# Performance work log

Hardware: AMD Instinct MI355X
Metric: run time of the kernel (lower is better)

The kernel has to match this reference:

```python
import jax, jax.numpy as jnp
import numpy as np

N = 10000          # nodes
E = 320000         # edges (~32 neighbors/node)
HID = 128          # hidden_channels
NF = 128           # num_filters
NG = 50            # num_gaussians
NB = 6             # num_interactions
CUT = 10.0         # cutoff


def ssp(x):
    # ShiftedSoftplus: softplus(x) - log(2)
    return jax.nn.softplus(x) - jnp.log(2.0).astype(x.dtype)


def setup_inputs() -> dict:
    key = jax.random.key(0)
    ks = jax.random.split(key, 16)
    z = jax.random.randint(ks[0], (N,), 0, 100)
    pos = jax.random.uniform(ks[1], (N, 3), dtype=jnp.float32) * 5.0  # box so d < cutoff
    row = jax.random.randint(ks[2], (E,), 0, N)
    off = jax.random.randint(ks[3], (E,), 1, N)  # avoid self-loops (radius_graph excludes them)
    col = (row + off) % N
    edge_index = jnp.stack([row, col], axis=0)
    nrm = lambda k, s: 0.1 * jax.random.normal(k, s, dtype=jnp.float32)
    return {
        "z": z,
        "pos": pos,
        "edge_index": edge_index,
        "emb": nrm(ks[4], (100, HID)),
        "mlp_w1": nrm(ks[5], (NB, NG, NF)),
        "mlp_b1": jnp.zeros((NB, NF), jnp.float32),
        "mlp_w2": nrm(ks[6], (NB, NF, NF)),
        "mlp_b2": jnp.zeros((NB, NF), jnp.float32),
        "cl1_w": nrm(ks[7], (NB, HID, NF)),
        "cl2_w": nrm(ks[8], (NB, NF, HID)),
        "cl2_b": jnp.zeros((NB, HID), jnp.float32),
        "lin_w": nrm(ks[9], (NB, HID, HID)),
        "lin_b": jnp.zeros((NB, HID), jnp.float32),
        "out_w1": nrm(ks[10], (HID, HID // 2)),
        "out_b1": jnp.zeros((HID // 2,), jnp.float32),
        "out_w2": nrm(ks[11], (HID // 2, 1)),
        "out_b2": jnp.zeros((1,), jnp.float32),
    }


def schnet_fwd(z, pos, edge_index, emb, mlp_w1, mlp_b1, mlp_w2, mlp_b2,
               cl1_w, cl2_w, cl2_b, lin_w, lin_b, out_w1, out_b1, out_w2, out_b2):
    row, col = edge_index[0], edge_index[1]  # j (source), i (target)
    d = jnp.linalg.norm(pos[row] - pos[col], axis=-1)  # [E]
    offsets = jnp.linspace(0.0, CUT, NG)
    coeff = -0.5 / (offsets[1] - offsets[0]) ** 2
    edge_attr = jnp.exp(coeff * (d[:, None] - offsets) ** 2)  # [E, NG]
    C = 0.5 * (jnp.cos(d * jnp.pi / CUT) + 1.0)  # cosine cutoff [E]
    h = emb[z]  # [N, HID]
    n = h.shape[0]
    for k in range(NB):
        # per-edge filter MLP
        W = ssp(edge_attr @ mlp_w1[k] + mlp_b1[k]) @ mlp_w2[k] + mlp_b2[k]
        W = W * C[:, None]  # [E, NF]
        x = h @ cl1_w[k]  # lin1 (no bias) [N, NF]
        msg = x[row] * W  # gather + modulate
        agg = jax.ops.segment_sum(msg, col, num_segments=n)  # scatter-add to targets
        x = agg @ cl2_w[k] + cl2_b[k]  # lin2 [N, HID]
        x = ssp(x)
        x = x @ lin_w[k] + lin_b[k]  # InteractionBlock.lin
        h = h + x  # residual
    h = ssp(h @ out_w1 + out_b1)
    return h @ out_w2 + out_b2  # [N, 1]


def reference(z, pos, edge_index, emb, mlp_w1, mlp_b1, mlp_w2, mlp_b2,
              cl1_w, cl2_w, cl2_b, lin_w, lin_b, out_w1, out_b1, out_w2, out_b2):
    return schnet_fwd(z, pos, edge_index, emb, mlp_w1, mlp_b1, mlp_w2, mlp_b2,
                      cl1_w, cl2_w, cl2_b, lin_w, lin_b, out_w1, out_b1, out_w2, out_b2)
```

## Files before the change

kernel.cpp:

```cpp
#include <hip/hip_runtime.h>
#include <math.h>

#define N_NODES 10000
#define N_EDGES 320000
#define HID 128
#define NF 128
#define NG 50
#define NB 6
#define SCAN_CH 40
#define WFRAG_PER_K 24576
#define NWF_PER_MAT 32768
#define TBL_M 2048
#define DMAX 8.6602540378f

typedef __attribute__((ext_vector_type(8))) short bf16x8;
typedef __attribute__((ext_vector_type(4))) float f32x4;
typedef __attribute__((ext_vector_type(4))) unsigned int u32x4;

__device__ __forceinline__ int pi_map(int f) {
  return (f & ~31) | ((f & 15) << 1) | ((f >> 4) & 1);
}
__device__ __forceinline__ int pinv_map(int g) {
  return (g & ~31) | ((g & 1) << 4) | ((g & 31) >> 1);
}

__device__ __forceinline__ unsigned short f2bf(float f) {
  unsigned u = __float_as_uint(f);
  u += 0x7FFFu + ((u >> 16) & 1u);
  return (unsigned short)(u >> 16);
}
__device__ __forceinline__ float bf2f(unsigned short s) {
  return __uint_as_float(((unsigned)s) << 16);
}
__device__ __forceinline__ unsigned pack2f(float a, float b) {
  return ((__float_as_uint(a) + 0x8000u) >> 16) |
         ((__float_as_uint(b) + 0x8000u) & 0xFFFF0000u);
}
__device__ __forceinline__ float ssp_fast(float x) {
  float t = __expf(-fabsf(x));
  return fmaxf(x, 0.0f) + __logf(1.0f + t) - 0.69314718055994530942f;
}

__global__ __launch_bounds__(256) void k_embed(const int* __restrict__ z,
                                               const float* __restrict__ emb,
                                               float* __restrict__ h) {
  int t = blockIdx.x * 256 + threadIdx.x;
  if (t >= N_NODES * HID) return;
  int i = t >> 7, c = t & 127;
  h[t] = emb[z[i] * HID + c];
}

__global__ __launch_bounds__(256) void k_hist(const int* __restrict__ col,
                                              int* __restrict__ count) {
  int e = blockIdx.x * 256 + threadIdx.x;
  if (e < N_EDGES) atomicAdd(&count[col[e]], 1);
}

__global__ __launch_bounds__(256) void k_scan(const int* __restrict__ count,
                                              int* __restrict__ rowptr,
                                              int* __restrict__ cursor) {
  __shared__ int s_part[256];
  int t = threadIdx.x;
  int begin = t * SCAN_CH, end = min(begin + SCAN_CH, N_NODES);
  int s = 0;
  for (int i = begin; i < end; i++) s += count[i];
  s_part[t] = s;
  __syncthreads();
  for (int off = 1; off < 256; off <<= 1) {
    int v = (t >= off) ? s_part[t - off] : 0;
    __syncthreads();
    s_part[t] += v;
    __syncthreads();
  }
  int run = (t > 0) ? s_part[t - 1] : 0;
  for (int i = begin; i < end; i++) {
    rowptr[i] = run;
    cursor[i] = run;
    run += count[i];
  }
  if (t == 255) rowptr[N_NODES] = N_EDGES;
}

__global__ __launch_bounds__(256) void k_scatter(const int* __restrict__ row,
                                                 const int* __restrict__ col,
                                                 const float* __restrict__ pos,
                                                 int* __restrict__ cursor,
                                                 int2* __restrict__ sorted_ru) {
  int e = blockIdx.x * 256 + threadIdx.x;
  if (e >= N_EDGES) return;
  int c = col[e], r = row[e];
  float dx = pos[3 * r + 0] - pos[3 * c + 0];
  float dy = pos[3 * r + 1] - pos[3 * c + 1];
  float dz = pos[3 * r + 2] - pos[3 * c + 2];
  float d = sqrtf(dx * dx + dy * dy + dz * dz);
  int p = atomicAdd(&cursor[c], 1);
  float u = d * ((float)(TBL_M - 1) / DMAX);
  sorted_ru[p] = make_int2(r, __float_as_int(u));
}

__global__ __launch_bounds__(256) void k_pack(const float* __restrict__ w1,
                                              const float* __restrict__ w2,
                                              unsigned short* __restrict__ wf) {
  const float* w1k = w1 + (size_t)blockIdx.x * NG * NF;
  const float* w2k = w2 + (size_t)blockIdx.x * NF * NF;
  unsigned short* wfk = wf + (size_t)blockIdx.x * WFRAG_PER_K;
  for (int inst = threadIdx.x; inst < 3072; inst += 256) {
    int fi = inst >> 8;
    int wv = (inst >> 6) & 3;
    int lane = inst & 63;
    int r16 = lane & 15, kgrp = lane >> 4;
    bf16x8 v;
#pragma unroll
    for (int j = 0; j < 8; ++j) {
      float val;
      if (fi < 4) {
        int ncol = wv * 32 + r16 + (fi >> 1) * 16;
        int k = (fi & 1) * 32 + kgrp * 8 + j;
        val = (k < NG) ? w1k[k * NF + ncol] : 0.f;
      } else {
        int fi2 = fi - 4;
        int ncol = wv * 32 + r16 + (fi2 >> 2) * 16;
        int kpi = (fi2 & 3) * 32 + kgrp * 8 + j;
        val = w2k[pinv_map(kpi) * NF + ncol];
      }
      v[j] = (short)f2bf(val);
    }
    *(bf16x8*)&wfk[inst * 8] = v;
  }
}

__global__ __launch_bounds__(256) void k_packn(const float* __restrict__ cl1,
                                               const float* __restrict__ cl2,
                                               const float* __restrict__ lin,
                                               unsigned short* __restrict__ nwf) {
  const int mat = blockIdx.x;
  const float* src = (mat < 6) ? cl1 + (size_t)mat * HID * NF
                   : (mat < 12) ? cl2 + (size_t)(mat - 6) * NF * HID
                                : lin + (size_t)(mat - 12) * HID * HID;
  unsigned short* dst = nwf + (size_t)mat * NWF_PER_MAT;
  for (int inst = threadIdx.x; inst < 2048; inst += 256) {
    int fi = inst >> 8;
    int wv = (inst >> 6) & 3;
    int lane = inst & 63;
    int r16 = lane & 15, kgrp = lane >> 4;
    int ncol = wv * 32 + r16 + (fi >> 2) * 16;
    int kb = fi & 3;
    bf16x8 fh, fl;
#pragma unroll
    for (int j = 0; j < 8; ++j) {
      float val = src[(kb * 32 + kgrp * 8 + j) * 128 + ncol];
      unsigned short hh = f2bf(val);
      fh[j] = (short)hh;
      fl[j] = (short)f2bf(val - bf2f(hh));
    }
    *(bf16x8*)&dst[((fi * 4 + wv) * 64 + lane) * 8] = fh;
    *(bf16x8*)&dst[(((fi + 8) * 4 + wv) * 64 + lane) * 8] = fl;
  }
}

__device__ __forceinline__ void stage_hilo(unsigned short* s_hi, unsigned short* s_lo,
                                           int rr, int c4, float4 v) {
  int cs = c4 ^ ((rr & 7) << 3);
  unsigned hax = (__float_as_uint(v.x) + 0x8000u) & 0xFFFF0000u;
  unsigned hay = (__float_as_uint(v.y) + 0x8000u) & 0xFFFF0000u;
  unsigned haz = (__float_as_uint(v.z) + 0x8000u) & 0xFFFF0000u;
  unsigned haw = (__float_as_uint(v.w) + 0x8000u) & 0xFFFF0000u;
  float lx = v.x - __uint_as_float(hax);
  float ly = v.y - __uint_as_float(hay);
  float lz = v.z - __uint_as_float(haz);
  float lw = v.w - __uint_as_float(haw);
  *(uint2*)&s_hi[rr * 128 + cs] = make_uint2((hax >> 16) | hay, (haz >> 16) | haw);
  *(uint2*)&s_lo[rr * 128 + cs] = make_uint2(pack2f(lx, ly), pack2f(lz, lw));
}

__device__ __forceinline__ int swz_idx(int row, int col) {
  return row * 128 + (((col & ~7) ^ ((row & 7) << 3)) | (col & 7));
}

#define KSTEP(accA, accB, kb, BH_A, BL_A, BH_B, BL_B, rowoff)                  \
  {                                                                            \
    bf16x8 ahi = *(const bf16x8*)&s_hi[(rowoff) + (((kb) * 32 + kb0) ^ swz)];  \
    bf16x8 alo = *(const bf16x8*)&s_lo[(rowoff) + (((kb) * 32 + kb0) ^ swz)];  \
    accA = __builtin_amdgcn_mfma_f32_16x16x32_bf16(ahi, BH_A, accA, 0, 0, 0);  \
    accA = __builtin_amdgcn_mfma_f32_16x16x32_bf16(alo, BH_A, accA, 0, 0, 0);  \
    accA = __builtin_amdgcn_mfma_f32_16x16x32_bf16(ahi, BL_A, accA, 0, 0, 0);  \
    accB = __builtin_amdgcn_mfma_f32_16x16x32_bf16(ahi, BH_B, accB, 0, 0, 0);  \
    accB = __builtin_amdgcn_mfma_f32_16x16x32_bf16(alo, BH_B, accB, 0, 0, 0);  \
    accB = __builtin_amdgcn_mfma_f32_16x16x32_bf16(ahi, BL_B, accB, 0, 0, 0);  \
  }
#define MFMA_ALL()                                          \
  {                                                         \
    const int ro0 = r16 * 128;                              \
    KSTEP(a00, a01, 0, bh00, bl00, bh10, bl10, ro0);        \
    KSTEP(a00, a01, 1, bh01, bl01, bh11, bl11, ro0);        \
    KSTEP(a00, a01, 2, bh02, bl02, bh12, bl12, ro0);        \
    KSTEP(a00, a01, 3, bh03, bl03, bh13, bl13, ro0);        \
    const int ro1 = (16 + r16) * 128;                       \
    KSTEP(a10, a11, 0, bh00, bl00, bh10, bl10, ro1);        \
    KSTEP(a10, a11, 1, bh01, bl01, bh11, bl11, ro1);        \
    KSTEP(a10, a11, 2, bh02, bl02, bh12, bl12, ro1);        \
    KSTEP(a10, a11, 3, bh03, bl03, bh13, bl13, ro1);        \
  }
#define LOAD_FRAGS(wfp)                                                              \
  const bf16x8* np = (const bf16x8*)(wfp);                                           \
  const bf16x8 bh00 = np[(0 * 4 + wvid) * 64 + lane], bh01 = np[(1 * 4 + wvid) * 64 + lane], \
               bh02 = np[(2 * 4 + wvid) * 64 + lane], bh03 = np[(3 * 4 + wvid) * 64 + lane], \
               bh10 = np[(4 * 4 + wvid) * 64 + lane], bh11 = np[(5 * 4 + wvid) * 64 + lane], \
               bh12 = np[(6 * 4 + wvid) * 64 + lane], bh13 = np[(7 * 4 + wvid) * 64 + lane], \
               bl00 = np[(8 * 4 + wvid) * 64 + lane], bl01 = np[(9 * 4 + wvid) * 64 + lane], \
               bl02 = np[(10 * 4 + wvid) * 64 + lane], bl03 = np[(11 * 4 + wvid) * 64 + lane], \
               bl10 = np[(12 * 4 + wvid) * 64 + lane], bl11 = np[(13 * 4 + wvid) * 64 + lane], \
               bl12 = np[(14 * 4 + wvid) * 64 + lane], bl13 = np[(15 * 4 + wvid) * 64 + lane];

__global__ __launch_bounds__(256) void k_ngemm(const float* __restrict__ in,
                                               const unsigned short* __restrict__ wf,
                                               float* __restrict__ out,
                                               int nrows) {
  __shared__ __align__(16) float s_buf[32 * 128];
  unsigned short* s_hi = (unsigned short*)s_buf;
  unsigned short* s_lo = s_hi + 32 * 128;
  float* s_out = s_buf;

  const int tid = threadIdx.x;
  const int lane = tid & 63;
  const int wvid = tid >> 6;
  const int r16 = lane & 15;
  const int kgrp = lane >> 4;
  const int kb0 = kgrp * 8;
  const int nc0 = wvid * 32 + r16;
  const int nc1 = nc0 + 16;
  const int r0 = blockIdx.x * 32;

#pragma unroll
  for (int j = 0; j < 4; ++j) {
    int idx4 = j * 256 + tid;
    int rr = idx4 >> 5;
    int c4 = (idx4 & 31) << 2;
    float4 v = make_float4(0.f, 0.f, 0.f, 0.f);
    if (r0 + rr < nrows) v = *(const float4*)&in[(size_t)(r0 + rr) * 128 + c4];
    stage_hilo(s_hi, s_lo, rr, c4, v);
  }
  LOAD_FRAGS(wf);
  __syncthreads();

  f32x4 a00 = {0.f, 0.f, 0.f, 0.f}, a01 = a00, a10 = a00, a11 = a00;
  const int swz = (r16 & 7) << 3;
  MFMA_ALL();
  __syncthreads();

#pragma unroll
  for (int r = 0; r < 4; ++r) {
    int er0 = kgrp * 4 + r, er1 = 16 + kgrp * 4 + r;
    s_out[er0 * 128 + (nc0 ^ ((er0 & 7) << 2))] = a00[r];
    s_out[er0 * 128 + (nc1 ^ ((er0 & 7) << 2))] = a01[r];
    s_out[er1 * 128 + (nc0 ^ ((er1 & 7) << 2))] = a10[r];
    s_out[er1 * 128 + (nc1 ^ ((er1 & 7) << 2))] = a11[r];
  }
  __syncthreads();

#pragma unroll
  for (int j = 0; j < 4; ++j) {
    int idx4 = j * 256 + tid;
    int rr = idx4 >> 5;
    int c4 = (idx4 & 31) << 2;
    if (r0 + rr >= nrows) continue;
    int cs = c4 ^ ((rr & 7) << 2);
    *(float4*)&out[(size_t)(r0 + rr) * 128 + c4] = *(float4*)&s_out[rr * 128 + cs];
  }
}

__global__ __launch_bounds__(256) void k_ngemm2(const float* __restrict__ agg,
                                                const unsigned short* __restrict__ wf_cl2,
                                                const float* __restrict__ b_cl2,
                                                const unsigned short* __restrict__ wf_lin,
                                                const float* __restrict__ b_lin,
                                                float* __restrict__ h,
                                                int nrows) {
  __shared__ __align__(16) float s_buf[32 * 128];
  unsigned short* s_hi = (unsigned short*)s_buf;
  unsigned short* s_lo = s_hi + 32 * 128;
  float* s_out = s_buf;

  const int tid = threadIdx.x;
  const int lane = tid & 63;
  const int wvid = tid >> 6;
  const int r16 = lane & 15;
  const int kgrp = lane >> 4;
  const int kb0 = kgrp * 8;
  const int nc0 = wvid * 32 + r16;
  const int nc1 = nc0 + 16;
  const int r0 = blockIdx.x * 32;
  const int swz = (r16 & 7) << 3;

#pragma unroll
  for (int j = 0; j < 4; ++j) {
    int idx4 = j * 256 + tid;
    int rr = idx4 >> 5;
    int c4 = (idx4 & 31) << 2;
    float4 v = make_float4(0.f, 0.f, 0.f, 0.f);
    if (r0 + rr < nrows) v = *(const float4*)&agg[(size_t)(r0 + rr) * 128 + c4];
    stage_hilo(s_hi, s_lo, rr, c4, v);
  }
  const float bc0 = b_cl2[nc0], bc1 = b_cl2[nc1];
  const float bl0_ = b_lin[nc0], bl1_ = b_lin[nc1];
  __syncthreads();

  f32x4 a00 = {0.f, 0.f, 0.f, 0.f}, a01 = a00, a10 = a00, a11 = a00;
  {
    LOAD_FRAGS(wf_cl2);
    MFMA_ALL();
  }
  __syncthreads();

#pragma unroll
  for (int r = 0; r < 4; ++r) {
    int er0 = kgrp * 4 + r, er1 = 16 + kgrp * 4 + r;
    float t00 = ssp_fast(a00[r] + bc0);
    float t01 = ssp_fast(a01[r] + bc1);
    float t10 = ssp_fast(a10[r] + bc0);
    float t11 = ssp_fast(a11[r] + bc1);
    unsigned u;
    u = (__float_as_uint(t00) + 0x8000u) & 0xFFFF0000u;
    s_hi[swz_idx(er0, nc0)] = (unsigned short)(u >> 16);
    s_lo[swz_idx(er0, nc0)] = (unsigned short)(pack2f(t00 - __uint_as_float(u), 0.f));
    u = (__float_as_uint(t01) + 0x8000u) & 0xFFFF0000u;
    s_hi[swz_idx(er0, nc1)] = (unsigned short)(u >> 16);
    s_lo[swz_idx(er0, nc1)] = (unsigned short)(pack2f(t01 - __uint_as_float(u), 0.f));
    u = (__float_as_uint(t10) + 0x8000u) & 0xFFFF0000u;
    s_hi[swz_idx(er1, nc0)] = (unsigned short)(u >> 16);
    s_lo[swz_idx(er1, nc0)] = (unsigned short)(pack2f(t10 - __uint_as_float(u), 0.f));
    u = (__float_as_uint(t11) + 0x8000u) & 0xFFFF0000u;
    s_hi[swz_idx(er1, nc1)] = (unsigned short)(u >> 16);
    s_lo[swz_idx(er1, nc1)] = (unsigned short)(pack2f(t11 - __uint_as_float(u), 0.f));
  }
  __syncthreads();

  f32x4 c00 = {0.f, 0.f, 0.f, 0.f}, c01 = c00, c10 = c00, c11 = c00;
  {
    LOAD_FRAGS(wf_lin);
    const int ro0 = r16 * 128;
    KSTEP(c00, c01, 0, bh00, bl00, bh10, bl10, ro0);
    KSTEP(c00, c01, 1, bh01, bl01, bh11, bl11, ro0);
    KSTEP(c00, c01, 2, bh02, bl02, bh12, bl12, ro0);
    KSTEP(c00, c01, 3, bh03, bl03, bh13, bl13, ro0);
    const int ro1 = (16 + r16) * 128;
    KSTEP(c10, c11, 0, bh00, bl00, bh10, bl10, ro1);
    KSTEP(c10, c11, 1, bh01, bl01, bh11, bl11, ro1);
    KSTEP(c10, c11, 2, bh02, bl02, bh12, bl12, ro1);
    KSTEP(c10, c11, 3, bh03, bl03, bh13, bl13, ro1);
  }
  __syncthreads();

#pragma unroll
  for (int r = 0; r < 4; ++r) {
    int er0 = kgrp * 4 + r, er1 = 16 + kgrp * 4 + r;
    s_out[er0 * 128 + (nc0 ^ ((er0 & 7) << 2))] = c00[r] + bl0_;
    s_out[er0 * 128 + (nc1 ^ ((er0 & 7) << 2))] = c01[r] + bl1_;
    s_out[er1 * 128 + (nc0 ^ ((er1 & 7) << 2))] = c10[r] + bl0_;
    s_out[er1 * 128 + (nc1 ^ ((er1 & 7) << 2))] = c11[r] + bl1_;
  }
  __syncthreads();

#pragma unroll
  for (int j = 0; j < 4; ++j) {
    int idx4 = j * 256 + tid;
    int rr = idx4 >> 5;
    int c4 = (idx4 & 31) << 2;
    if (r0 + rr >= nrows) continue;
    int cs = c4 ^ ((rr & 7) << 2);
    float4 v = *(float4*)&s_out[rr * 128 + cs];
    float* dst = &h[(size_t)(r0 + rr) * 128 + c4];
    float4 o = *(const float4*)dst;
    v.x += o.x; v.y += o.y; v.z += o.z; v.w += o.w;
    *(float4*)dst = v;
  }
}

__global__ __launch_bounds__(256) void k_ngemm3(const float* __restrict__ agg,
                                                const unsigned short* __restrict__ wf_cl2,
                                                const float* __restrict__ b_cl2,
                                                const unsigned short* __restrict__ wf_lin,
                                                const float* __restrict__ b_lin,
                                                const unsigned short* __restrict__ wf_cl1n,
                                                float* __restrict__ h,
                                                float* __restrict__ x,
                                                int nrows) {
  __shared__ __align__(16) float s_buf[32 * 128];
  unsigned short* s_hi = (unsigned short*)s_buf;
  unsigned short* s_lo = s_hi + 32 * 128;
  float* s_out = s_buf;

  const int tid = threadIdx.x;
  const int lane = tid & 63;
  const int wvid = tid >> 6;
  const int r16 = lane & 15;
  const int kgrp = lane >> 4;
  const int kb0 = kgrp * 8;
  const int nc0 = wvid * 32 + r16;
  const int nc1 = nc0 + 16;
  const int r0 = blockIdx.x * 32;
  const int swz = (r16 & 7) << 3;

#pragma unroll
  for (int j = 0; j < 4; ++j) {
    int idx4 = j * 256 + tid;
    int rr = idx4 >> 5;
    int c4 = (idx4 & 31) << 2;
    float4 v = make_float4(0.f, 0.f, 0.f, 0.f);
    if (r0 + rr < nrows) v = *(const float4*)&agg[(size_t)(r0 + rr) * 128 + c4];
    stage_hilo(s_hi, s_lo, rr, c4, v);
  }
  const float bc0 = b_cl2[nc0], bc1 = b_cl2[nc1];
  const float bl0_ = b_lin[nc0], bl1_ = b_lin[nc1];
  __syncthreads();

  f32x4 a00 = {0.f, 0.f, 0.f, 0.f}, a01 = a00, a10 = a00, a11 = a00;
  {
    LOAD_FRAGS(wf_cl2);
    MFMA_ALL();
  }
  __syncthreads();

#pragma unroll
  for (int r = 0; r < 4; ++r) {
    int er0 = kgrp * 4 + r, er1 = 16 + kgrp * 4 + r;
    float t00 = ssp_fast(a00[r] + bc0);
    float t01 = ssp_fast(a01[r] + bc1);
    float t10 = ssp_fast(a10[r] + bc0);
    float t11 = ssp_fast(a11[r] + bc1);
    unsigned u;
    u = (__float_as_uint(t00) + 0x8000u) & 0xFFFF0000u;
    s_hi[swz_idx(er0, nc0)] = (unsigned short)(u >> 16);
    s_lo[swz_idx(er0, nc0)] = (unsigned short)(pack2f(t00 - __uint_as_float(u), 0.f));
    u = (__float_as_uint(t01) + 0x8000u) & 0xFFFF0000u;
    s_hi[swz_idx(er0, nc1)] = (unsigned short)(u >> 16);
    s_lo[swz_idx(er0, nc1)] = (unsigned short)(pack2f(t01 - __uint_as_float(u), 0.f));
    u = (__float_as_uint(t10) + 0x8000u) & 0xFFFF0000u;
    s_hi[swz_idx(er1, nc0)] = (unsigned short)(u >> 16);
    s_lo[swz_idx(er1, nc0)] = (unsigned short)(pack2f(t10 - __uint_as_float(u), 0.f));
    u = (__float_as_uint(t11) + 0x8000u) & 0xFFFF0000u;
    s_hi[swz_idx(er1, nc1)] = (unsigned short)(u >> 16);
    s_lo[swz_idx(er1, nc1)] = (unsigned short)(pack2f(t11 - __uint_as_float(u), 0.f));
  }
  __syncthreads();

  f32x4 c00 = {0.f, 0.f, 0.f, 0.f}, c01 = c00, c10 = c00, c11 = c00;
  {
    LOAD_FRAGS(wf_lin);
    const int ro0 = r16 * 128;
    KSTEP(c00, c01, 0, bh00, bl00, bh10, bl10, ro0);
    KSTEP(c00, c01, 1, bh01, bl01, bh11, bl11, ro0);
    KSTEP(c00, c01, 2, bh02, bl02, bh12, bl12, ro0);
    KSTEP(c00, c01, 3, bh03, bl03, bh13, bl13, ro0);
    const int ro1 = (16 + r16) * 128;
    KSTEP(c10, c11, 0, bh00, bl00, bh10, bl10, ro1);
    KSTEP(c10, c11, 1, bh01, bl01, bh11, bl11, ro1);
    KSTEP(c10, c11, 2, bh02, bl02, bh12, bl12, ro1);
    KSTEP(c10, c11, 3, bh03, bl03, bh13, bl13, ro1);
  }
  __syncthreads();

#pragma unroll
  for (int r = 0; r < 4; ++r) {
    int er0 = kgrp * 4 + r, er1 = 16 + kgrp * 4 + r;
    s_out[er0 * 128 + (nc0 ^ ((er0 & 7) << 2))] = c00[r] + bl0_;
    s_out[er0 * 128 + (nc1 ^ ((er0 & 7) << 2))] = c01[r] + bl1_;
    s_out[er1 * 128 + (nc0 ^ ((er1 & 7) << 2))] = c10[r] + bl0_;
    s_out[er1 * 128 + (nc1 ^ ((er1 & 7) << 2))] = c11[r] + bl1_;
  }
  __syncthreads();

  float4 vv[4];
#pragma unroll
  for (int j = 0; j < 4; ++j) {
    int idx4 = j * 256 + tid;
    int rr = idx4 >> 5;
    int c4 = (idx4 & 31) << 2;
    int cs = c4 ^ ((rr & 7) << 2);
    float4 v = *(float4*)&s_out[rr * 128 + cs];
    if (r0 + rr < nrows) {
      float4 o = *(const float4*)&h[(size_t)(r0 + rr) * 128 + c4];
      v.x += o.x; v.y += o.y; v.z += o.z; v.w += o.w;
    } else {
      v = make_float4(0.f, 0.f, 0.f, 0.f);
    }
    vv[j] = v;
  }
  __syncthreads();
#pragma unroll
  for (int j = 0; j < 4; ++j) {
    int idx4 = j * 256 + tid;
    int rr = idx4 >> 5;
    int c4 = (idx4 & 31) << 2;
    stage_hilo(s_hi, s_lo, rr, c4, vv[j]);
    if (r0 + rr < nrows) *(float4*)&h[(size_t)(r0 + rr) * 128 + c4] = vv[j];
  }
  __syncthreads();

  a00 = (f32x4){0.f, 0.f, 0.f, 0.f}; a01 = a00; a10 = a00; a11 = a00;
  {
    LOAD_FRAGS(wf_cl1n);
    MFMA_ALL();
  }
  __syncthreads();

#pragma unroll
  for (int r = 0; r < 4; ++r) {
    int er0 = kgrp * 4 + r, er1 = 16 + kgrp * 4 + r;
    s_out[er0 * 128 + (nc0 ^ ((er0 & 7) << 2))] = a00[r];
    s_out[er0 * 128 + (nc1 ^ ((er0 & 7) << 2))] = a01[r];
    s_out[er1 * 128 + (nc0 ^ ((er1 & 7) << 2))] = a10[r];
    s_out[er1 * 128 + (nc1 ^ ((er1 & 7) << 2))] = a11[r];
  }
  __syncthreads();

#pragma unroll
  for (int j = 0; j < 4; ++j) {
    int idx4 = j * 256 + tid;
    int rr = idx4 >> 5;
    int c4 = (idx4 & 31) << 2;
    if (r0 + rr >= nrows) continue;
    int cs = c4 ^ ((rr & 7) << 2);
    *(float4*)&x[(size_t)(r0 + rr) * 128 + c4] = *(float4*)&s_out[rr * 128 + cs];
  }
}

__global__ __launch_bounds__(256) void k_tbuild(
    const unsigned short* __restrict__ wf_all, const float* __restrict__ b1_all,
    const float* __restrict__ b2_all, float* __restrict__ T_all) {
  __shared__ __align__(16) unsigned short s_rbf[128 * 64];
  __shared__ __align__(16) unsigned short s_t1[128 * 128];
  __shared__ float s_C[128];

  const int kk = blockIdx.x >> 4;
  const int sb = blockIdx.x & 15;
  const int s0 = sb * 128;
  const unsigned short* wf = wf_all + (size_t)kk * WFRAG_PER_K;
  const float* b1 = b1_all + (size_t)kk * NF;
  const float* b2 = b2_all + (size_t)kk * NF;
  float* T = T_all + (size_t)kk * TBL_M * NF;

  const int tid = threadIdx.x;
  const int lane = tid & 63;
  const int wvid = tid >> 6;
  const int r16 = lane & 15;
  const int kgrp = lane >> 4;
  const int kb0 = kgrp * 8;
  const int nc0 = wvid * 32 + r16;
  const int nc1 = nc0 + 16;
  const int pcol = wvid * 32 + 2 * r16;

  const bf16x8* wp = (const bf16x8*)wf;
#define FR(fi) wp[((fi) * 4 + wvid) * 64 + lane]
  const bf16x8 w1_00 = FR(0), w1_10 = FR(1), w1_01 = FR(2), w1_11 = FR(3);
  const bf16x8 w2_00 = FR(4), w2_10 = FR(5), w2_20 = FR(6), w2_30 = FR(7);
  const bf16x8 w2_01 = FR(8), w2_11 = FR(9), w2_21 = FR(10), w2_31 = FR(11);
#undef FR
  const float b1n0 = b1[nc0], b1n1 = b1[nc1];
  const float b2n0 = b2[nc0], b2n1 = b2[nc1];

  {
    const int e = tid >> 1, gh = tid & 1;
    const float d = (float)(s0 + e) * (DMAX / (float)(TBL_M - 1));
    if (gh == 0) s_C[e] = 0.5f * (__cosf(d * 0.31415926535897932f) + 1.0f);
    const float step = 10.0f / 49.0f;
    const float coeff = -0.5f / (step * step);
    const int swz = (e & 7) << 3;
#pragma unroll
    for (int o = 0; o < 4; ++o) {
      int g0 = gh * 32 + o * 8;
      float vv[8];
#pragma unroll
      for (int j = 0; j < 8; ++j) {
        int g = g0 + j;
        float t = d - step * (float)g;
        vv[j] = (g < NG) ? __expf(coeff * t * t) : 0.0f;
      }
      u32x4 pk;
      pk[0] = pack2f(vv[0], vv[1]);
      pk[1] = pack2f(vv[2], vv[3]);
      pk[2] = pack2f(vv[4], vv[5]);
      pk[3] = pack2f(vv[6], vv[7]);
      *(u32x4*)&s_rbf[e * 64 + (g0 ^ swz)] = pk;
    }
  }
  __syncthreads();

  {
    const int swz = (r16 & 7) << 3;
    for (int mt = 0; mt < 8; ++mt) {
      const unsigned short* rp = &s_rbf[(mt * 16 + r16) * 64];
      bf16x8 a0 = *(const bf16x8*)&rp[(0 + kb0) ^ swz];
      bf16x8 a1 = *(const bf16x8*)&rp[(32 + kb0) ^ swz];
      f32x4 ac0 = {0.f, 0.f, 0.f, 0.f};
      f32x4 ac1 = {0.f, 0.f, 0.f, 0.f};
      ac0 = __builtin_amdgcn_mfma_f32_16x16x32_bf16(a0, w1_00, ac0, 0, 0, 0);
      ac0 = __builtin_amdgcn_mfma_f32_16x16x32_bf16(a1, w1_10, ac0, 0, 0, 0);
      ac1 = __builtin_amdgcn_mfma_f32_16x16x32_bf16(a0, w1_01, ac1, 0, 0, 0);
      ac1 = __builtin_amdgcn_mfma_f32_16x16x32_bf16(a1, w1_11, ac1, 0, 0, 0);
#pragma unroll
      for (int r = 0; r < 4; ++r) {
        int er = mt * 16 + kgrp * 4 + r;
        float v0 = ssp_fast(ac0[r] + b1n0);
        float v1 = ssp_fast(ac1[r] + b1n1);
        *(unsigned*)&s_t1[er * 128 + (pcol ^ ((er & 7) << 3))] = pack2f(v0, v1);
      }
    }
  }
  __syncthreads();

  {
    const int swz = (r16 & 7) << 3;
    for (int mt = 0; mt < 8; ++mt) {
      const unsigned short* tp = &s_t1[(mt * 16 + r16) * 128];
      bf16x8 a0 = *(const bf16x8*)&tp[(0 + kb0) ^ swz];
      bf16x8 a1 = *(const bf16x8*)&tp[(32 + kb0) ^ swz];
      bf16x8 a2 = *(const bf16x8*)&tp[(64 + kb0) ^ swz];
      bf16x8 a3 = *(const bf16x8*)&tp[(96 + kb0) ^ swz];
      f32x4 ac0 = {0.f, 0.f, 0.f, 0.f};
      f32x4 ac1 = {0.f, 0.f, 0.f, 0.f};
      ac0 = __builtin_amdgcn_mfma_f32_16x16x32_bf16(a0, w2_00, ac0, 0, 0, 0);
      ac0 = __builtin_amdgcn_mfma_f32_16x16x32_bf16(a1, w2_10, ac0, 0, 0, 0);
      ac0 = __builtin_amdgcn_mfma_f32_16x16x32_bf16(a2, w2_20, ac0, 0, 0, 0);
      ac0 = __builtin_amdgcn_mfma_f32_16x16x32_bf16(a3, w2_30, ac0, 0, 0, 0);
      ac1 = __builtin_amdgcn_mfma_f32_16x16x32_bf16(a0, w2_01, ac1, 0, 0, 0);
      ac1 = __builtin_amdgcn_mfma_f32_16x16x32_bf16(a1, w2_11, ac1, 0, 0, 0);
      ac1 = __builtin_amdgcn_mfma_f32_16x16x32_bf16(a2, w2_21, ac1, 0, 0, 0);
      ac1 = __builtin_amdgcn_mfma_f32_16x16x32_bf16(a3, w2_31, ac1, 0, 0, 0);
#pragma unroll
      for (int r = 0; r < 4; ++r) {
        int er = mt * 16 + kgrp * 4 + r;
        float Cc = s_C[er];
        float2 v = make_float2((ac0[r] + b2n0) * Cc, (ac1[r] + b2n1) * Cc);
        *(float2*)&T[(size_t)(s0 + er) * NF + pcol] = v;
      }
    }
  }
}

__global__ __launch_bounds__(256) void k_tpack(const float* __restrict__ T_all,
                                               unsigned* __restrict__ Tp_all) {
  size_t t = (size_t)blockIdx.x * 256 + threadIdx.x;
  int f = (int)(t & 127);
  size_t rem = t >> 7;
  int i = (int)(rem & (TBL_M - 1));
  int kk = (int)(rem >> 11);
  const float* T = T_all + (size_t)kk * TBL_M * NF;
  int pf = pi_map(f);
  float lo = T[(size_t)i * NF + pf];
  float hi = T[(size_t)min(i + 1, TBL_M - 1) * NF + pf];
  Tp_all[t] = pack2f(lo, hi);
}

__global__ __launch_bounds__(256) void k_aggr(const int2* __restrict__ ru,
                                              const int* __restrict__ rowptr,
                                              const unsigned* __restrict__ Tp,
                                              const float* __restrict__ x,
                                              float* __restrict__ agg) {
  __shared__ int2 s_ru[256];
  __shared__ float s_part[3 * 128];
  const int tid = threadIdx.x;
  const int wvid = tid >> 6;
  const int lane = tid & 63;
  const int f2 = lane * 2;
  const int n = blockIdx.x;
  const int beg = rowptr[n], end = rowptr[n + 1];

  float ax0 = 0.f, ay0 = 0.f, ax1 = 0.f, ay1 = 0.f;
  for (int cs = beg; cs < end; cs += 256) {
    const int cnt = min(256, end - cs);
    if (tid < cnt) s_ru[tid] = ru[cs + tid];
    __syncthreads();
    int j = wvid;
    for (; j + 4 < cnt; j += 8) {
      int2 p0 = s_ru[j];
      int2 p1 = s_ru[j + 4];
      float u0 = __int_as_float(p0.y), u1 = __int_as_float(p1.y);
      int i0 = min((int)u0, TBL_M - 2), i1 = min((int)u1, TBL_M - 2);
      float fr0 = u0 - (float)i0, fr1 = u1 - (float)i1;
      uint2 t0 = *(const uint2*)&Tp[(size_t)i0 * NF + f2];
      uint2 t1 = *(const uint2*)&Tp[(size_t)i1 * NF + f2];
      float2 x0 = *(const float2*)&x[(size_t)p0.x * NF + f2];
      float2 x1 = *(const float2*)&x[(size_t)p1.x * NF + f2];
      float lo, hi;
      lo = __uint_as_float(t0.x << 16); hi = __uint_as_float(t0.x & 0xFFFF0000u);
      ax0 = fmaf(fmaf(fr0, hi - lo, lo), x0.x, ax0);
      lo = __uint_as_float(t0.y << 16); hi = __uint_as_float(t0.y & 0xFFFF0000u);
      ay0 = fmaf(fmaf(fr0, hi - lo, lo), x0.y, ay0);
      lo = __uint_as_float(t1.x << 16); hi = __uint_as_float(t1.x & 0xFFFF0000u);
      ax1 = fmaf(fmaf(fr1, hi - lo, lo), x1.x, ax1);
      lo = __uint_as_float(t1.y << 16); hi = __uint_as_float(t1.y & 0xFFFF0000u);
      ay1 = fmaf(fmaf(fr1, hi - lo, lo), x1.y, ay1);
    }
    for (; j < cnt; j += 4) {
      int2 p0 = s_ru[j];
      float u0 = __int_as_float(p0.y);
      int i0 = min((int)u0, TBL_M - 2);
      float fr0 = u0 - (float)i0;
      uint2 t0 = *(const uint2*)&Tp[(size_t)i0 * NF + f2];
      float2 x0 = *(const float2*)&x[(size_t)p0.x * NF + f2];
      float lo, hi;
      lo = __uint_as_float(t0.x << 16); hi = __uint_as_float(t0.x & 0xFFFF0000u);
      ax0 = fmaf(fmaf(fr0, hi - lo, lo), x0.x, ax0);
      lo = __uint_as_float(t0.y << 16); hi = __uint_as_float(t0.y & 0xFFFF0000u);
      ay0 = fmaf(fmaf(fr0, hi - lo, lo), x0.y, ay0);
    }
    __syncthreads();
  }

  float fx = ax0 + ax1, fy = ay0 + ay1;
  if (wvid > 0) {
    *(float2*)&s_part[(wvid - 1) * 128 + f2] = make_float2(fx, fy);
  }
  __syncthreads();
  if (wvid == 0) {
#pragma unroll
    for (int w = 0; w < 3; ++w) {
      fx += s_part[w * 128 + f2];
      fy += s_part[w * 128 + f2 + 1];
    }
    *(float2*)&agg[(size_t)n * NF + f2] = make_float2(fx, fy);
  }
}

__global__ __launch_bounds__(256) void k_out(const float* __restrict__ h,
                                             const float* __restrict__ w1,
                                             const float* __restrict__ b1,
                                             const float* __restrict__ w2,
                                             const float* __restrict__ b2,
                                             float* __restrict__ out) {
  int wid = threadIdx.x >> 6;
  int lane = threadIdx.x & 63;
  int i = blockIdx.x * 4 + wid;
  if (i >= N_NODES) return;
  const float* __restrict__ hr = h + i * HID;
  float acc = b1[lane];
#pragma unroll 8
  for (int k = 0; k < HID; k++) acc = fmaf(hr[k], w1[k * 64 + lane], acc);
  float p = ssp_fast(acc) * w2[lane];
#pragma unroll
  for (int off = 32; off; off >>= 1) p += __shfl_down(p, off);
  if (lane == 0) out[i] = p + b2[0];
}

extern "C" void kernel_launch(void* const* d_in, const int* in_sizes, int n_in,
                              void* d_out, int out_size, void* d_ws, size_t ws_size,
                              hipStream_t stream) {
  const int* z = (const int*)d_in[0];
  const float* pos = (const float*)d_in[1];
  const int* eidx = (const int*)d_in[2];
  const float* emb = (const float*)d_in[3];
  const float* mlp_w1 = (const float*)d_in[4];
  const float* mlp_b1 = (const float*)d_in[5];
  const float* mlp_w2 = (const float*)d_in[6];
  const float* mlp_b2 = (const float*)d_in[7];
  const float* cl1_w = (const float*)d_in[8];
  const float* cl2_w = (const float*)d_in[9];
  const float* cl2_b = (const float*)d_in[10];
  const float* lin_w = (const float*)d_in[11];
  const float* lin_b = (const float*)d_in[12];
  const float* out_w1 = (const float*)d_in[13];
  const float* out_b1 = (const float*)d_in[14];
  const float* out_w2 = (const float*)d_in[15];
  const float* out_b2 = (const float*)d_in[16];
  float* out = (float*)d_out;

  float* h = (float*)d_ws;
  float* x = h + N_NODES * HID;
  float* agg = x + N_NODES * HID;
  int* count = (int*)(agg + N_NODES * HID);
  int* rowptr = count + 10240;
  int* cursor = rowptr + 10240;
  int2* sorted_ru = (int2*)(cursor + 10240);
  unsigned short* wfrag = (unsigned short*)(sorted_ru + N_EDGES);
  unsigned short* nwf = wfrag + (size_t)NB * WFRAG_PER_K;
  float* Tbl = (float*)(nwf + (size_t)18 * NWF_PER_MAT);
  unsigned* Tp = (unsigned*)(Tbl + (size_t)NB * TBL_M * NF);
  const int* row = eidx;
  const int* col = eidx + N_EDGES;

  hipMemsetAsync(count, 0, 10240 * sizeof(int), stream);
  k_hist<<<(N_EDGES + 255) / 256, 256, 0, stream>>>(col, count);
  k_scan<<<1, 256, 0, stream>>>(count, rowptr, cursor);
  k_scatter<<<(N_EDGES + 255) / 256, 256, 0, stream>>>(row, col, pos, cursor,
                                                       sorted_ru);

  k_pack<<<NB, 256, 0, stream>>>(mlp_w1, mlp_w2, wfrag);
  k_packn<<<18, 256, 0, stream>>>(cl1_w, cl2_w, lin_w, nwf);
  k_tbuild<<<NB * 16, 256, 0, stream>>>(wfrag, mlp_b1, mlp_b2, Tbl);
  k_tpack<<<(NB * TBL_M * NF) / 256, 256, 0, stream>>>(Tbl, Tp);

  k_embed<<<(N_NODES * HID + 255) / 256, 256, 0, stream>>>(z, emb, h);

  const int NGB = (N_NODES + 31) / 32;
  k_ngemm<<<NGB, 256, 0, stream>>>(h, nwf + (size_t)0 * NWF_PER_MAT, x, N_NODES);
  for (int k = 0; k < NB; k++) {
    k_aggr<<<N_NODES, 256, 0, stream>>>(sorted_ru, rowptr,
                                        Tp + (size_t)k * TBL_M * NF, x, agg);
    if (k < NB - 1) {
      k_ngemm3<<<NGB, 256, 0, stream>>>(
          agg, nwf + (size_t)(6 + k) * NWF_PER_MAT, cl2_b + (size_t)k * HID,
          nwf + (size_t)(12 + k) * NWF_PER_MAT, lin_b + (size_t)k * HID,
          nwf + (size_t)(k + 1) * NWF_PER_MAT, h, x, N_NODES);
    } else {
      k_ngemm2<<<NGB, 256, 0, stream>>>(
          agg, nwf + (size_t)(6 + k) * NWF_PER_MAT, cl2_b + (size_t)k * HID,
          nwf + (size_t)(12 + k) * NWF_PER_MAT, lin_b + (size_t)k * HID, h, N_NODES);
    }
  }

  k_out<<<(N_NODES + 3) / 4, 256, 0, stream>>>(h, out_w1, out_b1, out_w2, out_b2, out);
}
```

Measured before the change: 360.0 us.

## Store node features as bf16 for edge gather and halve GEMM row tiles

The lin1 output x is now written as packed bf16 pairs instead of fp32, so the per-edge gather in the aggregation kernel reads half the bytes per neighbour. Separately, the node GEMM kernels now process 16 rows per block instead of 32, which doubles the grid size for more parallelism across CUs. The trade-off is lower precision in the gathered features, and each block reloads the weight fragments for fewer rows.

Result: faster. 320.3 us (-11.0%).

```diff
diff --git a/kernel.cpp b/kernel.cpp
--- a/kernel.cpp
+++ b/kernel.cpp
@@ -177,10 +177,10 @@
   return row * 128 + (((col & ~7) ^ ((row & 7) << 3)) | (col & 7));
 }
 
-#define KSTEP(accA, accB, kb, BH_A, BL_A, BH_B, BL_B, rowoff)                  \
+#define KSTEP(accA, accB, kb, BH_A, BL_A, BH_B, BL_B)                          \
   {                                                                            \
-    bf16x8 ahi = *(const bf16x8*)&s_hi[(rowoff) + (((kb) * 32 + kb0) ^ swz)];  \
-    bf16x8 alo = *(const bf16x8*)&s_lo[(rowoff) + (((kb) * 32 + kb0) ^ swz)];  \
+    bf16x8 ahi = *(const bf16x8*)&s_hi[r16 * 128 + (((kb) * 32 + kb0) ^ swz)]; \
+    bf16x8 alo = *(const bf16x8*)&s_lo[r16 * 128 + (((kb) * 32 + kb0) ^ swz)]; \
     accA = __builtin_amdgcn_mfma_f32_16x16x32_bf16(ahi, BH_A, accA, 0, 0, 0);  \
     accA = __builtin_amdgcn_mfma_f32_16x16x32_bf16(alo, BH_A, accA, 0, 0, 0);  \
     accA = __builtin_amdgcn_mfma_f32_16x16x32_bf16(ahi, BL_A, accA, 0, 0, 0);  \
@@ -188,18 +188,12 @@
     accB = __builtin_amdgcn_mfma_f32_16x16x32_bf16(alo, BH_B, accB, 0, 0, 0);  \
     accB = __builtin_amdgcn_mfma_f32_16x16x32_bf16(ahi, BL_B, accB, 0, 0, 0);  \
   }
-#define MFMA_ALL()                                          \
-  {                                                         \
-    const int ro0 = r16 * 128;                              \
-    KSTEP(a00, a01, 0, bh00, bl00, bh10, bl10, ro0);        \
-    KSTEP(a00, a01, 1, bh01, bl01, bh11, bl11, ro0);        \
-    KSTEP(a00, a01, 2, bh02, bl02, bh12, bl12, ro0);        \
-    KSTEP(a00, a01, 3, bh03, bl03, bh13, bl13, ro0);        \
-    const int ro1 = (16 + r16) * 128;                       \
-    KSTEP(a10, a11, 0, bh00, bl00, bh10, bl10, ro1);        \
-    KSTEP(a10, a11, 1, bh01, bl01, bh11, bl11, ro1);        \
-    KSTEP(a10, a11, 2, bh02, bl02, bh12, bl12, ro1);        \
-    KSTEP(a10, a11, 3, bh03, bl03, bh13, bl13, ro1);        \
+#define MFMA_HALF(A0, A1)                          \
+  {                                                \
+    KSTEP(A0, A1, 0, bh00, bl00, bh10, bl10);      \
+    KSTEP(A0, A1, 1, bh01, bl01, bh11, bl11);      \
+    KSTEP(A0, A1, 2, bh02, bl02, bh12, bl12);      \
+    KSTEP(A0, A1, 3, bh03, bl03, bh13, bl13);      \
   }
 #define LOAD_FRAGS(wfp)                                                              \
   const bf16x8* np = (const bf16x8*)(wfp);                                           \
@@ -214,11 +208,11 @@
 
 __global__ __launch_bounds__(256) void k_ngemm(const float* __restrict__ in,
                                                const unsigned short* __restrict__ wf,
-                                               float* __restrict__ out,
+                                               unsigned* __restrict__ xb,
                                                int nrows) {
-  __shared__ __align__(16) float s_buf[32 * 128];
+  __shared__ __align__(16) float s_buf[16 * 128];
   unsigned short* s_hi = (unsigned short*)s_buf;
-  unsigned short* s_lo = s_hi + 32 * 128;
+  unsigned short* s_lo = s_hi + 16 * 128;
   float* s_out = s_buf;
 
   const int tid = threadIdx.x;
@@ -229,10 +223,10 @@
   const int kb0 = kgrp * 8;
   const int nc0 = wvid * 32 + r16;
   const int nc1 = nc0 + 16;
-  const int r0 = blockIdx.x * 32;
-
-#pragma unroll
-  for (int j = 0; j < 4; ++j) {
+  const int r0 = blockIdx.x * 16;
+
+#pragma unroll
+  for (int j = 0; j < 2; ++j) {
     int idx4 = j * 256 + tid;
     int rr = idx4 >> 5;
     int c4 = (idx4 & 31) << 2;
@@ -243,29 +237,29 @@
   LOAD_FRAGS(wf);
   __syncthreads();
 
-  f32x4 a00 = {0.f, 0.f, 0.f, 0.f}, a01 = a00, a10 = a00, a11 = a00;
+  f32x4 a00 = {0.f, 0.f, 0.f, 0.f}, a01 = a00;
   const int swz = (r16 & 7) << 3;
-  MFMA_ALL();
+  MFMA_HALF(a00, a01);
   __syncthreads();
 
 #pragma unroll
   for (int r = 0; r < 4; ++r) {
-    int er0 = kgrp * 4 + r, er1 = 16 + kgrp * 4 + r;
+    int er0 = kgrp * 4 + r;
     s_out[er0 * 128 + (nc0 ^ ((er0 & 7) << 2))] = a00[r];
     s_out[er0 * 128 + (nc1 ^ ((er0 & 7) << 2))] = a01[r];
-    s_out[er1 * 128 + (nc0 ^ ((er1 & 7) << 2))] = a10[r];
-    s_out[er1 * 128 + (nc1 ^ ((er1 & 7) << 2))] = a11[r];
-  }
-  __syncthreads();
-
-#pragma unroll
-  for (int j = 0; j < 4; ++j) {
+  }
+  __syncthreads();
+
+#pragma unroll
+  for (int j = 0; j < 2; ++j) {
     int idx4 = j * 256 + tid;
     int rr = idx4 >> 5;
     int c4 = (idx4 & 31) << 2;
     if (r0 + rr >= nrows) continue;
     int cs = c4 ^ ((rr & 7) << 2);
-    *(float4*)&out[(size_t)(r0 + rr) * 128 + c4] = *(float4*)&s_out[rr * 128 + cs];
+    float4 v = *(float4*)&s_out[rr * 128 + cs];
+    uint2 pk = make_uint2(pack2f(v.x, v.y), pack2f(v.z, v.w));
+    *(uint2*)&xb[(size_t)(r0 + rr) * 64 + (c4 >> 1)] = pk;
   }
 }
 
@@ -276,9 +270,9 @@
                                                 const float* __restrict__ b_lin,
                                                 float* __restrict__ h,
                                                 int nrows) {
-  __shared__ __align__(16) float s_buf[32 * 128];
+  __shared__ __align__(16) float s_buf[16 * 128];
   unsigned short* s_hi = (unsigned short*)s_buf;
-  unsigned short* s_lo = s_hi + 32 * 128;
+  unsigned short* s_lo = s_hi + 16 * 128;
   float* s_out = s_buf;
 
   const int tid = threadIdx.x;
@@ -289,11 +283,11 @@
   const int kb0 = kgrp * 8;
   const int nc0 = wvid * 32 + r16;
   const int nc1 = nc0 + 16;
-  const int r0 = blockIdx.x * 32;
+  const int r0 = blockIdx.x * 16;
   const int swz = (r16 & 7) << 3;
 
 #pragma unroll
-  for (int j = 0; j < 4; ++j) {
+  for (int j = 0; j < 2; ++j) {
     int idx4 = j * 256 + tid;
     int rr = idx4 >> 5;
     int c4 = (idx4 & 31) << 2;
@@ -305,20 +299,18 @@
   const float bl0_ = b_lin[nc0], bl1_ = b_lin[nc1];
   __syncthreads();
 
-  f32x4 a00 = {0.f, 0.f, 0.f, 0.f}, a01 = a00, a10 = a00, a11 = a00;
+  f32x4 a00 = {0.f, 0.f, 0.f, 0.f}, a01 = a00;
   {
     LOAD_FRAGS(wf_cl2);
-    MFMA_ALL();
+    MFMA_HALF(a00, a01);
   }
   __syncthreads();
 
 #pragma unroll
   for (int r = 0; r < 4; ++r) {
-    int er0 = kgrp * 4 + r, er1 = 16 + kgrp * 4 + r;
+    int er0 = kgrp * 4 + r;
     float t00 = ssp_fast(a00[r] + bc0);
     float t01 = ssp_fast(a01[r] + bc1);
-    float t10 = ssp_fast(a10[r] + bc0);
-    float t11 = ssp_fast(a11[r] + bc1);
     unsigned u;
     u = (__float_as_uint(t00) + 0x8000u) & 0xFFFF0000u;
     s_hi[swz_idx(er0, nc0)] = (unsigned short)(u >> 16);
@@ -326,43 +318,26 @@
     u = (__float_as_uint(t01) + 0x8000u) & 0xFFFF0000u;
     s_hi[swz_idx(er0, nc1)] = (unsigned short)(u >> 16);
     s_lo[swz_idx(er0, nc1)] = (unsigned short)(pack2f(t01 - __uint_as_float(u), 0.f));
-    u = (__float_as_uint(t10) + 0x8000u) & 0xFFFF0000u;
-    s_hi[swz_idx(er1, nc0)] = (unsigned short)(u >> 16);
-    s_lo[swz_idx(er1, nc0)] = (unsigned short)(pack2f(t10 - __uint_as_float(u), 0.f));
-    u = (__float_as_uint(t11) + 0x8000u) & 0xFFFF0000u;
-    s_hi[swz_idx(er1, nc1)] = (unsigned short)(u >> 16);
-    s_lo[swz_idx(er1, nc1)] = (unsigned short)(pack2f(t11 - __uint_as_float(u), 0.f));
-  }
-  __syncthreads();
-
-  f32x4 c00 = {0.f, 0.f, 0.f, 0.f}, c01 = c00, c10 = c00, c11 = c00;
+  }
+  __syncthreads();
+
+  f32x4 c00 = {0.f, 0.f, 0.f, 0.f}, c01 = c00;
   {
     LOAD_FRAGS(wf_lin);
-    const int ro0 = r16 * 128;
-    KSTEP(c00, c01, 0, bh00, bl00, bh10, bl10, ro0);
-    KSTEP(c00, c01, 1, bh01, bl01, bh11, bl11, ro0);
-    KSTEP(c00, c01, 2, bh02, bl02, bh12, bl12, ro0);
-    KSTEP(c00, c01, 3, bh03, bl03, bh13, bl13, ro0);
-    const int ro1 = (16 + r16) * 128;
-    KSTEP(c10, c11, 0, bh00, bl00, bh10, bl10, ro1);
-    KSTEP(c10, c11, 1, bh01, bl01, bh11, bl11, ro1);
-    KSTEP(c10, c11, 2, bh02, bl02, bh12, bl12, ro1);
-    KSTEP(c10, c11, 3, bh03, bl03, bh13, bl13, ro1);
+    MFMA_HALF(c00, c01);
   }
   __syncthreads();
 
 #pragma unroll
   for (int r = 0; r < 4; ++r) {
-    int er0 = kgrp * 4 + r, er1 = 16 + kgrp * 4 + r;
+    int er0 = kgrp * 4 + r;
     s_out[er0 * 128 + (nc0 ^ ((er0 & 7) << 2))] = c00[r] + bl0_;
     s_out[er0 * 128 + (nc1 ^ ((er0 & 7) << 2))] = c01[r] + bl1_;
-    s_out[er1 * 128 + (nc0 ^ ((er1 & 7) << 2))] = c10[r] + bl0_;
-    s_out[er1 * 128 + (nc1 ^ ((er1 & 7) << 2))] = c11[r] + bl1_;
-  }
-  __syncthreads();
-
-#pragma unroll
-  for (int j = 0; j < 4; ++j) {
+  }
+  __syncthreads();
+
+#pragma unroll
+  for (int j = 0; j < 2; ++j) {
     int idx4 = j * 256 + tid;
     int rr = idx4 >> 5;
     int c4 = (idx4 & 31) << 2;
@@ -383,11 +358,11 @@
                                                 const float* __restrict__ b_lin,
                                                 const unsigned short* __restrict__ wf_cl1n,
                                                 float* __restrict__ h,
-                                                float* __restrict__ x,
+                                                unsigned* __restrict__ xb,
                                                 int nrows) {
-  __shared__ __align__(16) float s_buf[32 * 128];
+  __shared__ __align__(16) float s_buf[16 * 128];
   unsigned short* s_hi = (unsigned short*)s_buf;
-  unsigned short* s_lo = s_hi + 32 * 128;
+  unsigned short* s_lo = s_hi + 16 * 128;
   float* s_out = s_buf;
 
   const int tid = threadIdx.x;
@@ -398,11 +373,11 @@
   const int kb0 = kgrp * 8;
   const int nc0 = wvid * 32 + r16;
   const int nc1 = nc0 + 16;
-  const int r0 = blockIdx.x * 32;
+  const int r0 = blockIdx.x * 16;
   const int swz = (r16 & 7) << 3;
 
 #pragma unroll
-  for (int j = 0; j < 4; ++j) {
+  for (int j = 0; j < 2; ++j) {
     int idx4 = j * 256 + tid;
     int rr = idx4 >> 5;
     int c4 = (idx4 & 31) << 2;
@@ -414,20 +389,18 @@
   const float bl0_ = b_lin[nc0], bl1_ = b_lin[nc1];
   __syncthreads();
 
-  f32x4 a00 = {0.f, 0.f, 0.f, 0.f}, a01 = a00, a10 = a00, a11 = a00;
+  f32x4 a00 = {0.f, 0.f, 0.f, 0.f}, a01 = a00;
   {
     LOAD_FRAGS(wf_cl2);
-    MFMA_ALL();
+    MFMA_HALF(a00, a01);
   }
   __syncthreads();
 
 #pragma unroll
   for (int r = 0; r < 4; ++r) {
-    int er0 = kgrp * 4 + r, er1 = 16 + kgrp * 4 + r;
+    int er0 = kgrp * 4 + r;
     float t00 = ssp_fast(a00[r] + bc0);
     float t01 = ssp_fast(a01[r] + bc1);
-    float t10 = ssp_fast(a10[r] + bc0);
-    float t11 = ssp_fast(a11[r] + bc1);
     unsigned u;
     u = (__float_as_uint(t00) + 0x8000u) & 0xFFFF0000u;
     s_hi[swz_idx(er0, nc0)] = (unsigned short)(u >> 16);
@@ -435,44 +408,27 @@
     u = (__float_as_uint(t01) + 0x8000u) & 0xFFFF0000u;
     s_hi[swz_idx(er0, nc1)] = (unsigned short)(u >> 16);
     s_lo[swz_idx(er0, nc1)] = (unsigned short)(pack2f(t01 - __uint_as_float(u), 0.f));
-    u = (__float_as_uint(t10) + 0x8000u) & 0xFFFF0000u;
-    s_hi[swz_idx(er1, nc0)] = (unsigned short)(u >> 16);
-    s_lo[swz_idx(er1, nc0)] = (unsigned short)(pack2f(t10 - __uint_as_float(u), 0.f));
-    u = (__float_as_uint(t11) + 0x8000u) & 0xFFFF0000u;
-    s_hi[swz_idx(er1, nc1)] = (unsigned short)(u >> 16);
-    s_lo[swz_idx(er1, nc1)] = (unsigned short)(pack2f(t11 - __uint_as_float(u), 0.f));
-  }
-  __syncthreads();
-
-  f32x4 c00 = {0.f, 0.f, 0.f, 0.f}, c01 = c00, c10 = c00, c11 = c00;
+  }
+  __syncthreads();
+
+  f32x4 c00 = {0.f, 0.f, 0.f, 0.f}, c01 = c00;
   {
     LOAD_FRAGS(wf_lin);
-    const int ro0 = r16 * 128;
-    KSTEP(c00, c01, 0, bh00, bl00, bh10, bl10, ro0);
-    KSTEP(c00, c01, 1, bh01, bl01, bh11, bl11, ro0);
-    KSTEP(c00, c01, 2, bh02, bl02, bh12, bl12, ro0);
-    KSTEP(c00, c01, 3, bh03, bl03, bh13, bl13, ro0);
-    const int ro1 = (16 + r16) * 128;
-    KSTEP(c10, c11, 0, bh00, bl00, bh10, bl10, ro1);
-    KSTEP(c10, c11, 1, bh01, bl01, bh11, bl11, ro1);
-    KSTEP(c10, c11, 2, bh02, bl02, bh12, bl12, ro1);
-    KSTEP(c10, c11, 3, bh03, bl03, bh13, bl13, ro1);
+    MFMA_HALF(c00, c01);
   }
   __syncthreads();
 
 #pragma unroll
   for (int r = 0; r < 4; ++r) {
-    int er0 = kgrp * 4 + r, er1 = 16 + kgrp * 4 + r;
+    int er0 = kgrp * 4 + r;
     s_out[er0 * 128 + (nc0 ^ ((er0 & 7) << 2))] = c00[r] + bl0_;
     s_out[er0 * 128 + (nc1 ^ ((er0 & 7) << 2))] = c01[r] + bl1_;
-    s_out[er1 * 128 + (nc0 ^ ((er1 & 7) << 2))] = c10[r] + bl0_;
-    s_out[er1 * 128 + (nc1 ^ ((er1 & 7) << 2))] = c11[r] + bl1_;
-  }
-  __syncthreads();
-
-  float4 vv[4];
-#pragma unroll
-  for (int j = 0; j < 4; ++j) {
+  }
+  __syncthreads();
+
+  float4 vv[2];
+#pragma unroll
+  for (int j = 0; j < 2; ++j) {
     int idx4 = j * 256 + tid;
     int rr = idx4 >> 5;
     int c4 = (idx4 & 31) << 2;
@@ -488,7 +444,7 @@
   }
   __syncthreads();
 #pragma unroll
-  for (int j = 0; j < 4; ++j) {
+  for (int j = 0; j < 2; ++j) {
     int idx4 = j * 256 + tid;
     int rr = idx4 >> 5;
     int c4 = (idx4 & 31) << 2;
@@ -497,31 +453,31 @@
   }
   __syncthreads();
 
-  a00 = (f32x4){0.f, 0.f, 0.f, 0.f}; a01 = a00; a10 = a00; a11 = a00;
+  a00 = (f32x4){0.f, 0.f, 0.f, 0.f}; a01 = a00;
   {
     LOAD_FRAGS(wf_cl1n);
-    MFMA_ALL();
+    MFMA_HALF(a00, a01);
   }
   __syncthreads();
 
 #pragma unroll
   for (int r = 0; r < 4; ++r) {
-    int er0 = kgrp * 4 + r, er1 = 16 + kgrp * 4 + r;
+    int er0 = kgrp * 4 + r;
     s_out[er0 * 128 + (nc0 ^ ((er0 & 7) << 2))] = a00[r];
     s_out[er0 * 128 + (nc1 ^ ((er0 & 7) << 2))] = a01[r];
-    s_out[er1 * 128 + (nc0 ^ ((er1 & 7) << 2))] = a10[r];
-    s_out[er1 * 128 + (nc1 ^ ((er1 & 7) << 2))] = a11[r];
-  }
-  __syncthreads();
-
-#pragma unroll
-  for (int j = 0; j < 4; ++j) {
+  }
+  __syncthreads();
+
+#pragma unroll
+  for (int j = 0; j < 2; ++j) {
     int idx4 = j * 256 + tid;
     int rr = idx4 >> 5;
     int c4 = (idx4 & 31) << 2;
     if (r0 + rr >= nrows) continue;
     int cs = c4 ^ ((rr & 7) << 2);
-    *(float4*)&x[(size_t)(r0 + rr) * 128 + c4] = *(float4*)&s_out[rr * 128 + cs];
+    float4 v = *(float4*)&s_out[rr * 128 + cs];
+    uint2 pk = make_uint2(pack2f(v.x, v.y), pack2f(v.z, v.w));
+    *(uint2*)&xb[(size_t)(r0 + rr) * 64 + (c4 >> 1)] = pk;
   }
 }
 
@@ -655,7 +611,7 @@
 __global__ __launch_bounds__(256) void k_aggr(const int2* __restrict__ ru,
                                               const int* __restrict__ rowptr,
                                               const unsigned* __restrict__ Tp,
-                                              const float* __restrict__ x,
+                                              const unsigned* __restrict__ xb,
                                               float* __restrict__ agg) {
   __shared__ int2 s_ru[256];
   __shared__ float s_part[3 * 128];
@@ -680,17 +636,17 @@
       float fr0 = u0 - (float)i0, fr1 = u1 - (float)i1;
       uint2 t0 = *(const uint2*)&Tp[(size_t)i0 * NF + f2];
       uint2 t1 = *(const uint2*)&Tp[(size_t)i1 * NF + f2];
-      float2 x0 = *(const float2*)&x[(size_t)p0.x * NF + f2];
-      float2 x1 = *(const float2*)&x[(size_t)p1.x * NF + f2];
+      unsigned xw0 = xb[(size_t)p0.x * 64 + lane];
+      unsigned xw1 = xb[(size_t)p1.x * 64 + lane];
       float lo, hi;
       lo = __uint_as_float(t0.x << 16); hi = __uint_as_float(t0.x & 0xFFFF0000u);
-      ax0 = fmaf(fmaf(fr0, hi - lo, lo), x0.x, ax0);
+      ax0 = fmaf(fmaf(fr0, hi - lo, lo), __uint_as_float(xw0 << 16), ax0);
       lo = __uint_as_float(t0.y << 16); hi = __uint_as_float(t0.y & 0xFFFF0000u);
-      ay0 = fmaf(fmaf(fr0, hi - lo, lo), x0.y, ay0);
+      ay0 = fmaf(fmaf(fr0, hi - lo, lo), __uint_as_float(xw0 & 0xFFFF0000u), ay0);
       lo = __uint_as_float(t1.x << 16); hi = __uint_as_float(t1.x & 0xFFFF0000u);
-      ax1 = fmaf(fmaf(fr1, hi - lo, lo), x1.x, ax1);
+      ax1 = fmaf(fmaf(fr1, hi - lo, lo), __uint_as_float(xw1 << 16), ax1);
       lo = __uint_as_float(t1.y << 16); hi = __uint_as_float(t1.y & 0xFFFF0000u);
-      ay1 = fmaf(fmaf(fr1, hi - lo, lo), x1.y, ay1);
+      ay1 = fmaf(fmaf(fr1, hi - lo, lo), __uint_as_float(xw1 & 0xFFFF0000u), ay1);
     }
     for (; j < cnt; j += 4) {
       int2 p0 = s_ru[j];
@@ -698,12 +654,12 @@
       int i0 = min((int)u0, TBL_M - 2);
       float fr0 = u0 - (float)i0;
       uint2 t0 = *(const uint2*)&Tp[(size_t)i0 * NF + f2];
-      float2 x0 = *(const float2*)&x[(size_t)p0.x * NF + f2];
+      unsigned xw0 = xb[(size_t)p0.x * 64 + lane];
       float lo, hi;
       lo = __uint_as_float(t0.x << 16); hi = __uint_as_float(t0.x & 0xFFFF0000u);
-      ax0 = fmaf(fmaf(fr0, hi - lo, lo), x0.x, ax0);
+      ax0 = fmaf(fmaf(fr0, hi - lo, lo), __uint_as_float(xw0 << 16), ax0);
       lo = __uint_as_float(t0.y << 16); hi = __uint_as_float(t0.y & 0xFFFF0000u);
-      ay0 = fmaf(fmaf(fr0, hi - lo, lo), x0.y, ay0);
+      ay0 = fmaf(fmaf(fr0, hi - lo, lo), __uint_as_float(xw0 & 0xFFFF0000u), ay0);
     }
     __syncthreads();
   }
@@ -766,9 +722,9 @@
   float* out = (float*)d_out;
 
   float* h = (float*)d_ws;
-  float* x = h + N_NODES * HID;
-  float* agg = x + N_NODES * HID;
-  int* count = (int*)(agg + N_NODES * HID);
+  float* agg = h + N_NODES * HID;
+  unsigned* xb = (unsigned*)(agg + N_NODES * HID);
+  int* count = (int*)(xb + N_NODES * 64);
   int* rowptr = count + 10240;
   int* cursor = rowptr + 10240;
   int2* sorted_ru = (int2*)(cursor + 10240);
@@ -792,16 +748,16 @@
 
   k_embed<<<(N_NODES * HID + 255) / 256, 256, 0, stream>>>(z, emb, h);
 
-  const int NGB = (N_NODES + 31) / 32;
-  k_ngemm<<<NGB, 256, 0, stream>>>(h, nwf + (size_t)0 * NWF_PER_MAT, x, N_NODES);
+  const int NGB = (N_NODES + 15) / 16;
+  k_ngemm<<<NGB, 256, 0, stream>>>(h, nwf + (size_t)0 * NWF_PER_MAT, xb, N_NODES);
   for (int k = 0; k < NB; k++) {
     k_aggr<<<N_NODES, 256, 0, stream>>>(sorted_ru, rowptr,
-                                        Tp + (size_t)k * TBL_M * NF, x, agg);
+                                        Tp + (size_t)k * TBL_M * NF, xb, agg);
     if (k < NB - 1) {
       k_ngemm3<<<NGB, 256, 0, stream>>>(
           agg, nwf + (size_t)(6 + k) * NWF_PER_MAT, cl2_b + (size_t)k * HID,
           nwf + (size_t)(12 + k) * NWF_PER_MAT, lin_b + (size_t)k * HID,
-          nwf + (size_t)(k + 1) * NWF_PER_MAT, h, x, N_NODES);
+          nwf + (size_t)(k + 1) * NWF_PER_MAT, h, xb, N_NODES);
     } else {
       k_ngemm2<<<NGB, 256, 0, stream>>>(
           agg, nwf + (size_t)(6 + k) * NWF_PER_MAT, cl2_b + (size_t)k * HID,
```
